# Optimization experiments

Hardware: AMD Instinct MI355X
Metric: run time of the kernel (lower is better)

The kernel has to match this reference:

```python
import jax, jax.numpy as jnp
import numpy as np
from jax import lax

IN_CH = 64
OUT_CH = 64
K = 3
CW = 2 * IN_CH + 49  # in_ch_weight = 2*in_ch + MAX_DISPLACEMENT**2 = 177
B = 8


def setup_inputs() -> dict:
    key = jax.random.key(0)
    ks = jax.random.split(key, 14)
    f = lambda k, s, sc: jax.random.normal(k, s, dtype=jnp.float32) * sc
    he5 = lambda cin: (2.0 / (cin * 25)) ** 0.5
    he3 = lambda cin: (2.0 / (cin * 9)) ** 0.5
    return {
        "x0": f(ks[0], (B, IN_CH, 128, 160), 1.0),
        "y0": f(ks[1], (B, IN_CH, 128, 160), 1.0),
        "x": f(ks[2], (B, IN_CH, 64, 80), 1.0),
        "y": f(ks[3], (B, IN_CH, 64, 80), 1.0),
        # weight-branch 0 (outputs CW channels)
        "w1a": f(ks[4], (IN_CH, CW, 5, 5), he5(CW)),
        "w1b": f(ks[5], (IN_CH, IN_CH, 5, 5), he5(IN_CH)),
        "w1c": f(ks[6], (CW, IN_CH, 3, 3), he3(IN_CH)),
        # weight-branch 1 / final (outputs OUT_CH channels)
        "w2a": f(ks[7], (IN_CH, CW, 5, 5), he5(CW)),
        "w2b": f(ks[8], (IN_CH, IN_CH, 5, 5), he5(IN_CH)),
        "w2c": f(ks[9], (OUT_CH, IN_CH, 3, 3), he3(IN_CH)),
        # grouped 1x1 dynamic-weight generators (per-channel affine maps)
        "wx_w": f(ks[10], (CW, CW * K * K), 0.05),
        "wx_b": f(ks[11], (CW, CW * K * K), 0.05),
        "wxf_w": f(ks[12], (OUT_CH, OUT_CH * K * K), 0.05),
        "wxf_b": f(ks[13], (OUT_CH, OUT_CH * K * K), 0.05),
    }


def _conv(x, w, stride, pad):
    return lax.conv_general_dilated(
        x, w, (stride, stride), [(pad, pad), (pad, pad)],
        dimension_numbers=("NCHW", "OIHW", "NCHW"))


def _pool2(x):
    b, c, h, w = x.shape
    return x.reshape(b, c, h // 2, 2, w // 2, 2).mean(axis=(3, 5))


def _corr(x0, y0):
    # FlowNet-style correlation: max_displacement=7, stride2=2 ->
    # displacements {-6,-4,-2,0,2,4,6}^2 = 49 channels; mean over C.
    b, c, h, w = x0.shape
    D = 6
    yp = jnp.pad(y0, ((0, 0), (0, 0), (D, D), (D, D)))
    outs = []
    for dy in range(-6, 7, 2):
        for dx in range(-6, 7, 2):
            ys = yp[:, :, D + dy:D + dy + h, D + dx:D + dx + w]
            outs.append(jnp.mean(x0 * ys, axis=1))
    return jnp.stack(outs, axis=1)  # [B, 49, H, W]


def _branch(feat, wa, wb, wc):
    h = jax.nn.relu(_conv(feat, wa, 2, 2))
    h = jax.nn.relu(_conv(h, wb, 2, 2))
    h = _conv(h, wc, 2, 1)
    return h.mean(axis=(2, 3))  # adaptive_avg_pool2d -> (1,1), squeezed: [B, Cout]


def _adaptive_conv(x, w, pad):
    # per-sample conv weights w: [B, Cout, Cin, k, k]
    def one(xb, wb):
        return _conv(xb[None], wb, 1, pad)[0]
    return jax.vmap(one)(x, w)


def reference(x0, y0, x, y, w1a, w1b, w1c, w2a, w2b, w2c, wx_w, wx_b, wxf_w, wxf_b):
    b = x.shape[0]
    x0p = _pool2(x0)
    y0p = _pool2(y0)
    corr = _corr(x0p, y0p)                      # [B, 49, H, W]
    feat = jnp.concatenate([corr, x, y], axis=1)  # [B, CW, H, W]

    # iteration 0 (N-1 = 1): generate per-sample [CW,CW,3,3] filters, apply
    fv = _branch(feat, w1a, w1b, w1c)           # [B, CW]
    wx = (fv[:, :, None] * wx_w[None] + wx_b[None]).reshape(b, CW, CW, K, K)
    feat = jax.nn.relu(_adaptive_conv(feat, wx, K // 2))

    # final: generate per-sample [OUT_CH,OUT_CH,3,3] filters and return them
    fv = _branch(feat, w2a, w2b, w2c)           # [B, OUT_CH]
    wxf = (fv[:, :, None] * wxf_w[None] + wxf_b[None]).reshape(b, OUT_CH, OUT_CH, K, K)
    return wxf
```

## Files before the change

kernel.cpp:

```cpp
#include <hip/hip_runtime.h>

typedef unsigned short u16;
typedef __attribute__((ext_vector_type(8))) short bf16x8;
typedef __attribute__((ext_vector_type(4))) float f32x4;
typedef _Float16 half2_t __attribute__((ext_vector_type(2)));

static constexpr int B  = 8;
static constexpr int C  = 64;
static constexpr int CW = 177;
static constexpr int H  = 64, W  = 80;
static constexpr int HP = 68, WP = 84, KC = 192;
static constexpr int PB = HP * WP * KC;
static constexpr int HA = 36, WA = 44;

__device__ __forceinline__ u16 f2b(float f) {
  union { float f; unsigned u; } v; v.f = f;
  unsigned u = v.u;
  return (u16)((u + 0x7FFF + ((u >> 16) & 1)) >> 16);
}
__device__ __forceinline__ u16 f2h(float f) {
  union { _Float16 h; u16 u; } v; v.h = (_Float16)f; return v.u;
}
__device__ __forceinline__ half2_t h2(unsigned u) {
  union { unsigned u; half2_t h; } v; v.u = u; return v.h;
}
__device__ __forceinline__ float blo(unsigned u) {
  union { unsigned v; float f; } t; t.v = u << 16; return t.f;
}
__device__ __forceinline__ float bhi(unsigned u) {
  union { unsigned v; float f; } t; t.v = u & 0xffff0000u; return t.f;
}
__device__ __forceinline__ unsigned pk2(u16 a, u16 b) {
  return (unsigned)a | ((unsigned)b << 16);
}

__global__ void setup_kernel(
    const float* __restrict__ w1a, const float* __restrict__ w2a,
    const float* __restrict__ w1b, const float* __restrict__ w2b,
    u16* __restrict__ A5a, u16* __restrict__ A5b,
    u16* __restrict__ A5b1, u16* __restrict__ A5b2,
    u16* __restrict__ featP1, u16* __restrict__ haP, u16* __restrict__ featP2) {
  int idx = blockIdx.x * blockDim.x + threadIdx.x;
  const int n0r = (B * PB) / 8;
  const int n1r = (B * HA * WA * 64) / 8;
  const int n2r = B * 592 * 24;
  const int s1 = 25 * 64 * 192, s2 = 25 * 64 * 64;
  bf16x8 z = 0;
  if (idx < n0r) { ((bf16x8*)featP1)[idx] = z; return; }
  idx -= n0r;
  if (idx < n1r) { ((bf16x8*)haP)[idx] = z; return; }
  idx -= n1r;
  if (idx < n2r) {
    int ch = idx % 24; int pi = (idx / 24) % 592; int b = idx / (24 * 592);
    int row, col;
    if (pi < 336) { int rr = pi / 84; row = (rr < 2) ? rr : rr + 64; col = pi % 84; }
    else { int pj = pi - 336; row = 2 + (pj >> 2); int cc = pj & 3; col = (cc < 2) ? cc : cc + 80; }
    *(bf16x8*)(featP2 + ((size_t)(b * HP + row) * WP + col) * KC + ch * 8) = z;
    return;
  }
  idx -= n2r;
  if (idx < 2 * s1) {
    const float* w = idx < s1 ? w1a : w2a; u16* A = idx < s1 ? A5a : A5b;
    int e = idx % s1;
    int j = e % 192; int i = (e / 192) % 64; int kk = e / (192 * 64);
    int ky = kk / 5, kx = kk % 5;
    float v = (j < CW) ? w[(((size_t)i * CW + j) * 5 + ky) * 5 + kx] : 0.f;
    A[e] = f2b(v);
    return;
  }
  idx -= 2 * s1;
  if (idx < 2 * s2) {
    const float* w = idx < s2 ? w1b : w2b; u16* A = idx < s2 ? A5b1 : A5b2;
    int e = idx % s2;
    int j = e % 64; int i = (e / 64) % 64; int kk = e / (64 * 64);
    int ky = kk / 5, kx = kk % 5;
    A[e] = f2b(w[(((size_t)i * 64 + j) * 5 + ky) * 5 + kx]);
  }
}

__global__ __launch_bounds__(256) void pool2_kernel(const float* __restrict__ x0, const float* __restrict__ y0,
                                                    u16* __restrict__ xpT, u16* __restrict__ ypT) {
  __shared__ u16 lt[80][66];
  int blk = blockIdx.x;
  int sel = blk & 1; int h = (blk >> 1) & 63; int b = blk >> 7;
  const float* in = sel ? y0 : x0;
  u16* out = sel ? ypT : xpT;
  int tid = threadIdx.x;
#pragma unroll
  for (int i = 0; i < 20; ++i) {
    int e = i * 256 + tid;
    int c = e / 80, w = e % 80;
    const float* p = in + ((size_t)(b * 64 + c) * 128 + 2 * h) * 160 + 2 * w;
    float2 r0 = *(const float2*)p;
    float2 r1 = *(const float2*)(p + 160);
    lt[w][c] = f2h(0.25f * (r0.x + r0.y + r1.x + r1.y));
  }
  __syncthreads();
#pragma unroll
  for (int i = 0; i < 20; ++i) {
    int e = i * 256 + tid;
    int w = e / 64, c = e % 64;
    out[((size_t)(b * H + h) * W + w) * C + c] = lt[w][c];
  }
}

__global__ __launch_bounds__(256) void corr_fill(const u16* __restrict__ xpT, const u16* __restrict__ ypT,
                                                 u16* __restrict__ featP) {
  int blk = blockIdx.x;
  int b = blk & 7; int inner = blk >> 3;
  int e = inner * 256 + threadIdx.x;
  int o = e % 49; int p = e / 49;
  int w = p % W; int h = p / W;
  int dy = (o / 7) * 2 - 6, dx = (o % 7) * 2 - 6;
  int hh = h + dy, ww = w + dx;
  float s = 0.f;
  if (hh >= 0 && hh < H && ww >= 0 && ww < W) {
    const uint4* xv = (const uint4*)(xpT + ((size_t)(b * H + h) * W + w) * C);
    const uint4* yv = (const uint4*)(ypT + ((size_t)(b * H + hh) * W + ww) * C);
#pragma unroll
    for (int i = 0; i < 8; ++i) {
      uint4 a = xv[i], q = yv[i];
      s = __builtin_amdgcn_fdot2(h2(a.x), h2(q.x), s, false);
      s = __builtin_amdgcn_fdot2(h2(a.y), h2(q.y), s, false);
      s = __builtin_amdgcn_fdot2(h2(a.z), h2(q.z), s, false);
      s = __builtin_amdgcn_fdot2(h2(a.w), h2(q.w), s, false);
    }
  }
  s *= (1.0f / 64.0f);
  featP[((size_t)(b * HP + h + 2) * WP + (w + 2)) * KC + o] = f2b(s);
}

__global__ __launch_bounds__(256) void copy_tr(const float* __restrict__ x, const float* __restrict__ y,
                                               u16* __restrict__ featP) {
  __shared__ float lt[40][129];
  int blk = blockIdx.x;
  int half = blk & 1; int h = (blk >> 1) & 63; int b = blk >> 7;
  int tid = threadIdx.x;
#pragma unroll
  for (int i = 0; i < 20; ++i) {
    int e = i * 256 + tid;
    int c2 = e / 40, w = e % 40;
    const float* src = (c2 < 64) ? x : y;
    int c = c2 & 63;
    lt[w][c2] = src[((size_t)(b * 64 + c) * H + h) * W + half * 40 + w];
  }
  __syncthreads();
#pragma unroll
  for (int i = 0; i < 20; ++i) {
    int e = i * 256 + tid;
    int wr = e / 128, c = e % 128;
    featP[((size_t)(b * HP + h + 2) * WP + (half * 40 + wr + 2)) * KC + 49 + c] = f2b(lt[wr][c]);
  }
}

__global__ void wx_pack(const float* __restrict__ fv, const float* __restrict__ ww,
                        const float* __restrict__ wb, u16* __restrict__ Apk) {
  int idx = blockIdx.x * blockDim.x + threadIdx.x;
  if (idx >= 9 * 192 * 24) return;
  int j8 = idx % 24; int i = (idx / 24) % 192; int kk = idx / (24 * 192);
  float wwv[8], wbv[8];
#pragma unroll
  for (int jj = 0; jj < 8; ++jj) {
    int j = j8 * 8 + jj;
    if (i < CW && j < CW) {
      size_t o = ((size_t)i * CW + j) * 9 + kk;
      wwv[jj] = ww[o]; wbv[jj] = wb[o];
    } else { wwv[jj] = 0.f; wbv[jj] = 0.f; }
  }
  int rb = i >> 4, il = i & 15;
  int c = j8 >> 3, rem = j8 & 7, half = rem >> 2, kqq = rem & 3;
  size_t dst = (((((size_t)kk * 12 + rb) * 3 + c) * 2 + half) * 64 + kqq * 16 + il) * 8;
  for (int b = 0; b < B; ++b) {
    float f = (i < CW) ? fv[b * CW + i] : 0.f;
    u16 o[8];
#pragma unroll
    for (int jj = 0; jj < 8; ++jj) o[jj] = f2b(f * wwv[jj] + wbv[jj]);
    uint4 v; v.x = pk2(o[0], o[1]); v.y = pk2(o[2], o[3]); v.z = pk2(o[4], o[5]); v.w = pk2(o[6], o[7]);
    *(uint4*)(Apk + (size_t)b * 331776 + dst) = v;
  }
}

__global__ __launch_bounds__(256, 2) void ad_conv_kernel(
    const u16* __restrict__ Apk, const u16* __restrict__ featP, u16* __restrict__ outP) {
  __shared__ u16 lds[2][84 * 64];
  int bid = (int)(blockIdx.x % 8) * 64 + (int)(blockIdx.x / 8);
  int h = bid & 63; int b = bid >> 6;
  int tid = threadIdx.x;
  int lane = tid & 63; int wm = tid >> 6;
  int l15 = lane & 15, kq = lane >> 4;

  f32x4 acc[3][5];
#pragma unroll
  for (int i = 0; i < 3; ++i)
#pragma unroll
    for (int j = 0; j < 5; ++j) acc[i][j] = (f32x4){0.f, 0.f, 0.f, 0.f};

  const u16* fb = featP + (size_t)b * PB;
  const u16* Ab = Apk + (size_t)b * 331776 + (size_t)lane * 8;

  int i0 = tid, i1 = tid + 256, i2 = tid + 512;
  int q0 = i0 >> 3, s0 = i0 & 7;
  int q1 = i1 >> 3, s1 = i1 & 7;
  int q2 = i2 >> 3, s2 = i2 & 7;
  int w0 = (i0 * 16) ^ ((q0 & 7) << 4);
  int w1 = (i1 * 16) ^ ((q1 & 7) << 4);
  int w2 = (i2 * 16) ^ ((q2 & 7) << 4);
  bool a2 = i2 < 672;

  bf16x8 r0, r1, r2;
  {
    const u16* g = fb + ((size_t)(h + 1) * WP) * KC;
    r0 = *(const bf16x8*)(g + (size_t)q0 * KC + s0 * 8);
    r1 = *(const bf16x8*)(g + (size_t)q1 * KC + s1 * 8);
    if (a2) r2 = *(const bf16x8*)(g + (size_t)q2 * KC + s2 * 8);
    char* lw = (char*)lds[0];
    *(bf16x8*)(lw + w0) = r0;
    *(bf16x8*)(lw + w1) = r1;
    if (a2) *(bf16x8*)(lw + w2) = r2;
  }
  __syncthreads();

#pragma unroll
  for (int s = 0; s < 9; ++s) {
    const int c = s / 3, ty = s % 3;
    if (s < 8) {
      const int cn = (s + 1) / 3, tyn = (s + 1) % 3;
      const u16* g = fb + ((size_t)(h + 1 + tyn) * WP) * KC + cn * 64;
      r0 = *(const bf16x8*)(g + (size_t)q0 * KC + s0 * 8);
      r1 = *(const bf16x8*)(g + (size_t)q1 * KC + s1 * 8);
      if (a2) r2 = *(const bf16x8*)(g + (size_t)q2 * KC + s2 * 8);
    }
    const char* lb = (const char*)lds[s & 1];
#pragma unroll
    for (int tx = 0; tx < 3; ++tx) {
      const int tap = ty * 3 + tx;
#pragma unroll
      for (int hk = 0; hk < 2; ++hk) {
        bf16x8 av[3], bv[5];
#pragma unroll
        for (int fm = 0; fm < 3; ++fm)
          av[fm] = *(const bf16x8*)(Ab + (size_t)(((tap * 12 + wm * 3 + fm) * 3 + c) * 2 + hk) * 512);
#pragma unroll
        for (int fn = 0; fn < 5; ++fn) {
          int q = fn * 16 + l15 + tx + 1;
          int byte = ((q * 8 + hk * 4 + kq) * 16) ^ ((q & 7) << 4);
          bv[fn] = *(const bf16x8*)(lb + byte);
        }
        __builtin_amdgcn_s_setprio(1);
#pragma unroll
        for (int fm = 0; fm < 3; ++fm)
#pragma unroll
          for (int fn = 0; fn < 5; ++fn)
            acc[fm][fn] = __builtin_amdgcn_mfma_f32_16x16x32_bf16(av[fm], bv[fn], acc[fm][fn], 0, 0, 0);
        __builtin_amdgcn_s_setprio(0);
      }
    }
    if (s < 8) {
      char* lw = (char*)lds[(s + 1) & 1];
      *(bf16x8*)(lw + w0) = r0;
      *(bf16x8*)(lw + w1) = r1;
      if (a2) *(bf16x8*)(lw + w2) = r2;
      __syncthreads();
    }
  }

#pragma unroll
  for (int fm = 0; fm < 3; ++fm) {
    int i0r = wm * 48 + fm * 16 + kq * 4;
#pragma unroll
    for (int fn = 0; fn < 5; ++fn) {
      int ow = fn * 16 + l15;
      u16* dst = outP + ((size_t)(b * HP + h + 2) * WP + (ow + 2)) * KC + i0r;
      uint2 pkv;
      pkv.x = pk2(f2b(fmaxf(acc[fm][fn][0], 0.f)), f2b(fmaxf(acc[fm][fn][1], 0.f)));
      pkv.y = pk2(f2b(fmaxf(acc[fm][fn][2], 0.f)), f2b(fmaxf(acc[fm][fn][3], 0.f)));
      *(uint2*)dst = pkv;
    }
  }
}

__global__ __launch_bounds__(128, 3) void conv5_split_kernel(
    const u16* __restrict__ A5, const u16* __restrict__ featP, u16* __restrict__ pa) {
  __shared__ u16 lds[2][84 * 64];
  int bid = (int)(blockIdx.x % 8) * 160 + (int)(blockIdx.x / 8);
  int rp = bid % 16; int ty = (bid / 16) % 5; int csel = (bid / 80) % 2; int b = bid / 160;
  int r0 = rp * 2;
  int kc0 = csel * 3;
  int tid = threadIdx.x;
  int lane = tid & 63; int wm = tid >> 6;
  int l15 = lane & 15, kq = lane >> 4;

  f32x4 acc[2][5];
#pragma unroll
  for (int i = 0; i < 2; ++i)
#pragma unroll
    for (int j = 0; j < 5; ++j) acc[i][j] = (f32x4){0.f, 0.f, 0.f, 0.f};

  const u16* fb = featP + (size_t)b * PB;
  int rowg0 = 2 * r0 + ty;

  bf16x8 r[6];
  auto load_chunk = [&](int kc) {
#pragma unroll
    for (int it = 0; it < 6; ++it) {
      int idx = it * 128 + tid;
      if (idx < 672) {
        int slot = idx & 3; int q = (idx >> 2) % 84; int row = idx / 336;
        r[it] = *(const bf16x8*)(fb + ((size_t)(rowg0 + 2 * row) * WP + q) * KC + kc * 32 + slot * 8);
      }
    }
  };
  auto write_chunk = [&](int buf) {
    char* lw = (char*)lds[buf];
#pragma unroll
    for (int it = 0; it < 6; ++it) {
      int idx = it * 128 + tid;
      if (idx < 672) {
        int q = (idx >> 2) % 84;
        int byte = (idx * 16) ^ ((q & 7) << 4);
        *(bf16x8*)(lw + byte) = r[it];
      }
    }
  };

  load_chunk(kc0);
  write_chunk(0);
  __syncthreads();

#pragma unroll
  for (int k = 0; k < 3; ++k) {
    int kc = kc0 + k;
    if (k < 2) load_chunk(kc + 1);
    const char* lb = (const char*)lds[k & 1];
#pragma unroll
    for (int tx = 0; tx < 5; ++tx) {
      bf16x8 av[2], bv[5];
#pragma unroll
      for (int fm = 0; fm < 2; ++fm)
        av[fm] = *(const bf16x8*)(A5 + ((size_t)((ty * 5 + tx) * 64 + wm * 32 + fm * 16 + l15)) * 192 + kc * 32 + kq * 8);
#pragma unroll
      for (int fn = 0; fn < 5; ++fn) {
        int p = fn * 16 + l15;
        int orow = p / 40, ocol = p % 40;
        int q = ocol * 2 + tx;
        int byte = (((orow * 84 + q) * 4 + kq) * 16) ^ ((q & 7) << 4);
        bv[fn] = *(const bf16x8*)(lb + byte);
      }
      __builtin_amdgcn_s_setprio(1);
#pragma unroll
      for (int fm = 0; fm < 2; ++fm)
#pragma unroll
        for (int fn = 0; fn < 5; ++fn)
          acc[fm][fn] = __builtin_amdgcn_mfma_f32_16x16x32_bf16(av[fm], bv[fn], acc[fm][fn], 0, 0, 0);
      __builtin_amdgcn_s_setprio(0);
    }
    if (k < 2) {
      write_chunk((k + 1) & 1);
      __syncthreads();
    }
  }
  int slot10 = csel * 5 + ty;
#pragma unroll
  for (int fm = 0; fm < 2; ++fm) {
    int oc0 = wm * 32 + fm * 16 + kq * 4;
#pragma unroll
    for (int fn = 0; fn < 5; ++fn) {
      int p = fn * 16 + l15;
      int orow = r0 + p / 40, ocol = p % 40;
      u16* dst = pa + (((((size_t)slot10 * B + b) * 32 + orow) * 40 + ocol) * 64) + oc0;
      uint2 pkv;
      pkv.x = pk2(f2b(acc[fm][fn][0]), f2b(acc[fm][fn][1]));
      pkv.y = pk2(f2b(acc[fm][fn][2]), f2b(acc[fm][fn][3]));
      *(uint2*)dst = pkv;
    }
  }
}

__global__ void combine10(const u16* __restrict__ pa, u16* __restrict__ haP) {
  int idx = blockIdx.x * blockDim.x + threadIdx.x;
  if (idx >= B * 32 * 40 * 8) return;
  int c8 = idx & 7; int t = idx >> 3;
  int ocol = t % 40; t /= 40; int orow = t % 32; int b = t / 32;
  float s[8];
#pragma unroll
  for (int k = 0; k < 8; ++k) s[k] = 0.f;
#pragma unroll
  for (int sl = 0; sl < 10; ++sl) {
    const u16* p = pa + ((((size_t)sl * B + b) * 32 + orow) * 40 + ocol) * 64 + c8 * 8;
    uint4 v = *(const uint4*)p;
    s[0] += blo(v.x); s[1] += bhi(v.x); s[2] += blo(v.y); s[3] += bhi(v.y);
    s[4] += blo(v.z); s[5] += bhi(v.z); s[6] += blo(v.w); s[7] += bhi(v.w);
  }
  uint4 o;
  o.x = pk2(f2b(fmaxf(s[0], 0.f)), f2b(fmaxf(s[1], 0.f)));
  o.y = pk2(f2b(fmaxf(s[2], 0.f)), f2b(fmaxf(s[3], 0.f)));
  o.z = pk2(f2b(fmaxf(s[4], 0.f)), f2b(fmaxf(s[5], 0.f)));
  o.w = pk2(f2b(fmaxf(s[6], 0.f)), f2b(fmaxf(s[7], 0.f)));
  *(uint4*)(haP + ((size_t)(b * HA + orow + 2) * WA + (ocol + 2)) * 64 + c8 * 8) = o;
}

template<int TY, int TX, int S, int OH, int OW, int M, int BM, int BN, int POFF,
         int KCIN, int HPIN, int WPIN>
__global__ __launch_bounds__(256) void gemm_conv(
    const u16* __restrict__ A, const u16* __restrict__ featP,
    float* __restrict__ outF, int MT, int NT) {
  constexpr int WM = BM / 2, WN = BN / 2, FM = WM / 16, FN = WN / 16;
  constexpr int NKC = KCIN / 32;
  int nwg = gridDim.x;
  int bid = (int)(blockIdx.x % 8) * (nwg / 8) + (int)(blockIdx.x / 8);
  int mt = bid % MT; int rest = bid / MT; int nt = rest % NT; int b = rest / NT;
  int lane = threadIdx.x & 63; int wv = threadIdx.x >> 6;
  int wm = wv >> 1, wn = wv & 1;
  int l15 = lane & 15, kq = lane >> 4;

  f32x4 acc[FM][FN];
#pragma unroll
  for (int i = 0; i < FM; ++i)
#pragma unroll
    for (int j = 0; j < FN; ++j) acc[i][j] = (f32x4){0.f, 0.f, 0.f, 0.f};

  const u16* Abase = A + (size_t)(mt * BM + wm * WM + l15) * KCIN + kq * 8;
  const u16* fb = featP + (size_t)b * (HPIN * WPIN * KCIN) + kq * 8;

  int ohh[FN], oww[FN];
#pragma unroll
  for (int fn = 0; fn < FN; ++fn) {
    int p = nt * BN + wn * WN + fn * 16 + l15;
    ohh[fn] = p / OW; oww[fn] = p % OW;
  }

  for (int kc = 0; kc < NKC; ++kc) {
    for (int ty = 0; ty < TY; ++ty)
      for (int tx = 0; tx < TX; ++tx) {
        const u16* At = Abase + (size_t)((ty * TX + tx) * M) * KCIN + kc * 32;
        bf16x8 av[FM], bv[FN];
#pragma unroll
        for (int fm = 0; fm < FM; ++fm)
          av[fm] = *(const bf16x8*)(At + fm * 16 * KCIN);
#pragma unroll
        for (int fn = 0; fn < FN; ++fn) {
          int hi = ohh[fn] * S + ty + POFF;
          int wi = oww[fn] * S + tx + POFF;
          bv[fn] = *(const bf16x8*)(fb + (size_t)(hi * WPIN + wi) * KCIN + kc * 32);
        }
#pragma unroll
        for (int fm = 0; fm < FM; ++fm)
#pragma unroll
          for (int fn = 0; fn < FN; ++fn)
            acc[fm][fn] = __builtin_amdgcn_mfma_f32_16x16x32_bf16(av[fm], bv[fn], acc[fm][fn], 0, 0, 0);
      }
  }

#pragma unroll
  for (int fm = 0; fm < FM; ++fm) {
    int oc0 = mt * BM + wm * WM + fm * 16 + kq * 4;
#pragma unroll
    for (int fn = 0; fn < FN; ++fn) {
#pragma unroll
      for (int r = 0; r < 4; ++r) {
        float v = fmaxf(acc[fm][fn][r], 0.f);
        outF[(((size_t)b * M + oc0 + r) * OH + ohh[fn]) * OW + oww[fn]] = v;
      }
    }
  }
}

__global__ void tapsum_kernel(const float* __restrict__ hb, float* __restrict__ Sm) {
  int b = blockIdx.x >> 6; int ic = blockIdx.x & 63; int lane = threadIdx.x;
  const float* p = hb + ((size_t)(b * 64 + ic)) * 320;
  float s[9];
#pragma unroll
  for (int t = 0; t < 9; ++t) s[t] = 0.f;
  for (int i = lane; i < 320; i += 64) {
    int ih = i / 20, iw = i % 20;
    float v = p[i];
#pragma unroll
    for (int ky = 0; ky < 3; ++ky) {
      int t2 = ih + 1 - ky;
      if (t2 < 0 || t2 > 14 || (t2 & 1)) continue;
#pragma unroll
      for (int kx = 0; kx < 3; ++kx) {
        int t3 = iw + 1 - kx;
        if (t3 < 0 || t3 > 18 || (t3 & 1)) continue;
        s[ky * 3 + kx] += v;
      }
    }
  }
#pragma unroll
  for (int t = 0; t < 9; ++t)
#pragma unroll
    for (int off = 32; off > 0; off >>= 1) s[t] += __shfl_down(s[t], off);
  if (lane == 0) {
#pragma unroll
    for (int t = 0; t < 9; ++t) Sm[(b * 64 + ic) * 9 + t] = s[t];
  }
}

__global__ void gemv_fv(const float* __restrict__ w3, const float* __restrict__ Sm,
                        float* __restrict__ fv, int OC) {
  int o = blockIdx.x % OC; int b = blockIdx.x / OC; int lane = threadIdx.x;
  const float* wp = w3 + ((size_t)o * 64 + lane) * 9;
  const float* sp = Sm + ((size_t)b * 64 + lane) * 9;
  float acc = 0.f;
#pragma unroll
  for (int t = 0; t < 9; ++t) acc += wp[t] * sp[t];
#pragma unroll
  for (int off = 32; off > 0; off >>= 1) acc += __shfl_down(acc, off);
  if (lane == 0) fv[b * OC + o] = acc * (1.0f / 80.0f);
}

__global__ void final_kernel(const float* __restrict__ fv, const float* __restrict__ ww,
                             const float* __restrict__ wb, float* __restrict__ out) {
  int idx = blockIdx.x * blockDim.x + threadIdx.x;
  if (idx >= B * 64 * 576) return;
  int kk = idx % 576; int i = (idx / 576) % 64; int b = idx / (576 * 64);
  out[idx] = fv[b * 64 + i] * ww[i * 576 + kk] + wb[i * 576 + kk];
}

extern "C" void kernel_launch(void* const* d_in, const int* in_sizes, int n_in,
                              void* d_out, int out_size, void* d_ws, size_t ws_size,
                              hipStream_t stream) {
  const float* x0    = (const float*)d_in[0];
  const float* y0    = (const float*)d_in[1];
  const float* x     = (const float*)d_in[2];
  const float* y     = (const float*)d_in[3];
  const float* w1a   = (const float*)d_in[4];
  const float* w1b   = (const float*)d_in[5];
  const float* w1c   = (const float*)d_in[6];
  const float* w2a   = (const float*)d_in[7];
  const float* w2b   = (const float*)d_in[8];
  const float* w2c   = (const float*)d_in[9];
  const float* wx_w  = (const float*)d_in[10];
  const float* wx_b  = (const float*)d_in[11];
  const float* wxf_w = (const float*)d_in[12];
  const float* wxf_b = (const float*)d_in[13];
  float* out = (float*)d_out;

  char* base = (char*)d_ws;
  size_t off = 0;
  auto take = [&](size_t bytes) -> char* {
    char* p = base + off; off += (bytes + 255) & ~(size_t)255; return p;
  };
  u16*   featP1 = (u16*)take((size_t)B * PB * 2);
  u16*   featP2 = (u16*)take((size_t)B * PB * 2);
  u16*   paAwx  = (u16*)take((size_t)10 * B * 32 * 40 * 64 * 2);
  u16*   pa     = paAwx;
  u16*   Apk    = paAwx;
  u16*   xpT    = paAwx;
  u16*   ypT    = paAwx + (size_t)B * H * W * C;
  u16*   A5a    = (u16*)take((size_t)25 * 64 * 192 * 2);
  u16*   A5b    = (u16*)take((size_t)25 * 64 * 192 * 2);
  u16*   A5b1   = (u16*)take((size_t)25 * 64 * 64 * 2);
  u16*   A5b2   = (u16*)take((size_t)25 * 64 * 64 * 2);
  u16*   haP    = (u16*)take((size_t)B * HA * WA * 64 * 2);
  float* hb     = (float*)take((size_t)B * 64 * 320 * 4);
  float* Sm     = (float*)take((size_t)B * 64 * 9 * 4);
  float* fv1    = (float*)take((size_t)B * CW * 4);
  float* fv2    = (float*)take((size_t)B * 64 * 4);
  if (off > ws_size) return;

  const int TB = 256;

  {
    int n = (B * PB) / 8 + (B * HA * WA * 64) / 8 + B * 592 * 24
          + 2 * 25 * 64 * 192 + 2 * 25 * 64 * 64;
    setup_kernel<<<(n + TB - 1) / TB, TB, 0, stream>>>(
        w1a, w2a, w1b, w2b, A5a, A5b, A5b1, A5b2, featP1, haP, featP2);
  }
  pool2_kernel<<<B * 64 * 2, TB, 0, stream>>>(x0, y0, xpT, ypT);
  corr_fill<<<8 * 980, TB, 0, stream>>>(xpT, ypT, featP1);
  copy_tr<<<B * 64 * 2, TB, 0, stream>>>(x, y, featP1);

  conv5_split_kernel<<<1280, 128, 0, stream>>>(A5a, featP1, pa);
  combine10<<<(B * 32 * 40 * 8 + TB - 1) / TB, TB, 0, stream>>>(pa, haP);
  gemm_conv<5, 5, 2, 16, 20, 64, 32, 32, 0, 64, HA, WA>
      <<<160, TB, 0, stream>>>(A5b1, haP, hb, 2, 10);
  tapsum_kernel<<<B * 64, 64, 0, stream>>>(hb, Sm);
  gemv_fv<<<B * CW, 64, 0, stream>>>(w1c, Sm, fv1, CW);

  wx_pack<<<(9 * 192 * 24 + TB - 1) / TB, TB, 0, stream>>>(fv1, wx_w, wx_b, Apk);
  ad_conv_kernel<<<64 * B, 256, 0, stream>>>(Apk, featP1, featP2);

  conv5_split_kernel<<<1280, 128, 0, stream>>>(A5b, featP2, pa);
  combine10<<<(B * 32 * 40 * 8 + TB - 1) / TB, TB, 0, stream>>>(pa, haP);
  gemm_conv<5, 5, 2, 16, 20, 64, 32, 32, 0, 64, HA, WA>
      <<<160, TB, 0, stream>>>(A5b2, haP, hb, 2, 10);
  tapsum_kernel<<<B * 64, 64, 0, stream>>>(hb, Sm);
  gemv_fv<<<B * 64, 64, 0, stream>>>(w2c, Sm, fv2, 64);

  final_kernel<<<(B * 64 * 576 + TB - 1) / TB, TB, 0, stream>>>(fv2, wxf_w, wxf_b, out);
}
```

Before: 201.9 us.

## Fuse small kernels and fold tap-sum into gemm epilogue via atomics

Merges pool2 into the setup kernel, and corr_fill with copy_tr, so each pair runs as one launch with block-index dispatch. The tapsum pass is replaced by atomic accumulation into Sm in the gemm_conv epilogue, with Sm zeroed in combine10, and the final gemv is fused with the output affine kernel. The aim is to cut launch count and the hb intermediate round-trip. The cost is atomic contention, nondeterministic summation order, and a dependency on zeroing Sm inside combine10. The epilogue also assumes FM=FN=1, which holds for the 32x32 tiles used.

```diff
diff --git a/kernel.cpp b/kernel.cpp
--- a/kernel.cpp
+++ b/kernel.cpp
@@ -34,13 +34,40 @@
   return (unsigned)a | ((unsigned)b << 16);
 }
 
-__global__ void setup_kernel(
+__global__ __launch_bounds__(256) void setup_pool(
+    const float* __restrict__ x0, const float* __restrict__ y0,
+    u16* __restrict__ xpT, u16* __restrict__ ypT,
     const float* __restrict__ w1a, const float* __restrict__ w2a,
     const float* __restrict__ w1b, const float* __restrict__ w2b,
     u16* __restrict__ A5a, u16* __restrict__ A5b,
     u16* __restrict__ A5b1, u16* __restrict__ A5b2,
     u16* __restrict__ featP1, u16* __restrict__ haP, u16* __restrict__ featP2) {
-  int idx = blockIdx.x * blockDim.x + threadIdx.x;
+  __shared__ u16 lt[80][66];
+  int blk0 = blockIdx.x;
+  int tid = threadIdx.x;
+  if (blk0 < 1024) {
+    int sel = blk0 & 1; int h = (blk0 >> 1) & 63; int b = blk0 >> 7;
+    const float* in = sel ? y0 : x0;
+    u16* out = sel ? ypT : xpT;
+#pragma unroll
+    for (int i = 0; i < 20; ++i) {
+      int e = i * 256 + tid;
+      int c = e / 80, w = e % 80;
+      const float* p = in + ((size_t)(b * 64 + c) * 128 + 2 * h) * 160 + 2 * w;
+      float2 r0 = *(const float2*)p;
+      float2 r1 = *(const float2*)(p + 160);
+      lt[w][c] = f2h(0.25f * (r0.x + r0.y + r1.x + r1.y));
+    }
+    __syncthreads();
+#pragma unroll
+    for (int i = 0; i < 20; ++i) {
+      int e = i * 256 + tid;
+      int w = e / 64, c = e % 64;
+      out[((size_t)(b * H + h) * W + w) * C + c] = lt[w][c];
+    }
+    return;
+  }
+  int idx = (blk0 - 1024) * 256 + tid;
   const int n0r = (B * PB) / 8;
   const int n1r = (B * HA * WA * 64) / 8;
   const int n2r = B * 592 * 24;
@@ -78,64 +105,40 @@
   }
 }
 
-__global__ __launch_bounds__(256) void pool2_kernel(const float* __restrict__ x0, const float* __restrict__ y0,
-                                                    u16* __restrict__ xpT, u16* __restrict__ ypT) {
-  __shared__ u16 lt[80][66];
-  int blk = blockIdx.x;
-  int sel = blk & 1; int h = (blk >> 1) & 63; int b = blk >> 7;
-  const float* in = sel ? y0 : x0;
-  u16* out = sel ? ypT : xpT;
+__global__ __launch_bounds__(256) void corr_copy(
+    const u16* __restrict__ xpT, const u16* __restrict__ ypT,
+    const float* __restrict__ x, const float* __restrict__ y,
+    u16* __restrict__ featP) {
+  __shared__ float smf[40 * 129];
+  int blk0 = blockIdx.x;
   int tid = threadIdx.x;
-#pragma unroll
-  for (int i = 0; i < 20; ++i) {
-    int e = i * 256 + tid;
-    int c = e / 80, w = e % 80;
-    const float* p = in + ((size_t)(b * 64 + c) * 128 + 2 * h) * 160 + 2 * w;
-    float2 r0 = *(const float2*)p;
-    float2 r1 = *(const float2*)(p + 160);
-    lt[w][c] = f2h(0.25f * (r0.x + r0.y + r1.x + r1.y));
-  }
-  __syncthreads();
-#pragma unroll
-  for (int i = 0; i < 20; ++i) {
-    int e = i * 256 + tid;
-    int w = e / 64, c = e % 64;
-    out[((size_t)(b * H + h) * W + w) * C + c] = lt[w][c];
-  }
-}
-
-__global__ __launch_bounds__(256) void corr_fill(const u16* __restrict__ xpT, const u16* __restrict__ ypT,
-                                                 u16* __restrict__ featP) {
-  int blk = blockIdx.x;
-  int b = blk & 7; int inner = blk >> 3;
-  int e = inner * 256 + threadIdx.x;
-  int o = e % 49; int p = e / 49;
-  int w = p % W; int h = p / W;
-  int dy = (o / 7) * 2 - 6, dx = (o % 7) * 2 - 6;
-  int hh = h + dy, ww = w + dx;
-  float s = 0.f;
-  if (hh >= 0 && hh < H && ww >= 0 && ww < W) {
-    const uint4* xv = (const uint4*)(xpT + ((size_t)(b * H + h) * W + w) * C);
-    const uint4* yv = (const uint4*)(ypT + ((size_t)(b * H + hh) * W + ww) * C);
-#pragma unroll
-    for (int i = 0; i < 8; ++i) {
-      uint4 a = xv[i], q = yv[i];
-      s = __builtin_amdgcn_fdot2(h2(a.x), h2(q.x), s, false);
-      s = __builtin_amdgcn_fdot2(h2(a.y), h2(q.y), s, false);
-      s = __builtin_amdgcn_fdot2(h2(a.z), h2(q.z), s, false);
-      s = __builtin_amdgcn_fdot2(h2(a.w), h2(q.w), s, false);
-    }
-  }
-  s *= (1.0f / 64.0f);
-  featP[((size_t)(b * HP + h + 2) * WP + (w + 2)) * KC + o] = f2b(s);
-}
-
-__global__ __launch_bounds__(256) void copy_tr(const float* __restrict__ x, const float* __restrict__ y,
-                                               u16* __restrict__ featP) {
-  __shared__ float lt[40][129];
-  int blk = blockIdx.x;
+  if (blk0 < 7840) {
+    int b = blk0 & 7; int inner = blk0 >> 3;
+    int e = inner * 256 + tid;
+    int o = e % 49; int p = e / 49;
+    int w = p % W; int h = p / W;
+    int dy = (o / 7) * 2 - 6, dx = (o % 7) * 2 - 6;
+    int hh = h + dy, ww = w + dx;
+    float s = 0.f;
+    if (hh >= 0 && hh < H && ww >= 0 && ww < W) {
+      const uint4* xv = (const uint4*)(xpT + ((size_t)(b * H + h) * W + w) * C);
+      const uint4* yv = (const uint4*)(ypT + ((size_t)(b * H + hh) * W + ww) * C);
+#pragma unroll
+      for (int i = 0; i < 8; ++i) {
+        uint4 a = xv[i], q = yv[i];
+        s = __builtin_amdgcn_fdot2(h2(a.x), h2(q.x), s, false);
+        s = __builtin_amdgcn_fdot2(h2(a.y), h2(q.y), s, false);
+        s = __builtin_amdgcn_fdot2(h2(a.z), h2(q.z), s, false);
+        s = __builtin_amdgcn_fdot2(h2(a.w), h2(q.w), s, false);
+      }
+    }
+    s *= (1.0f / 64.0f);
+    featP[((size_t)(b * HP + h + 2) * WP + (w + 2)) * KC + o] = f2b(s);
+    return;
+  }
+  int blk = blk0 - 7840;
+  float (*lt)[129] = (float(*)[129])smf;
   int half = blk & 1; int h = (blk >> 1) & 63; int b = blk >> 7;
-  int tid = threadIdx.x;
 #pragma unroll
   for (int i = 0; i < 20; ++i) {
     int e = i * 256 + tid;
@@ -376,8 +379,10 @@
   }
 }
 
-__global__ void combine10(const u16* __restrict__ pa, u16* __restrict__ haP) {
+__global__ void combine10(const u16* __restrict__ pa, u16* __restrict__ haP,
+                          float* __restrict__ Sm) {
   int idx = blockIdx.x * blockDim.x + threadIdx.x;
+  if (idx < B * 64 * 9) Sm[idx] = 0.f;
   if (idx >= B * 32 * 40 * 8) return;
   int c8 = idx & 7; int t = idx >> 3;
   int ocol = t % 40; t /= 40; int orow = t % 32; int b = t / 32;
@@ -401,9 +406,9 @@
 
 template<int TY, int TX, int S, int OH, int OW, int M, int BM, int BN, int POFF,
          int KCIN, int HPIN, int WPIN>
-__global__ __launch_bounds__(256) void gemm_conv(
+__global__ __launch_bounds__(256) void gemm_conv_ts(
     const u16* __restrict__ A, const u16* __restrict__ featP,
-    float* __restrict__ outF, int MT, int NT) {
+    float* __restrict__ Sm, int MT, int NT) {
   constexpr int WM = BM / 2, WN = BN / 2, FM = WM / 16, FN = WN / 16;
   constexpr int NKC = KCIN / 32;
   int nwg = gridDim.x;
@@ -451,48 +456,27 @@
       }
   }
 
-#pragma unroll
-  for (int fm = 0; fm < FM; ++fm) {
-    int oc0 = mt * BM + wm * WM + fm * 16 + kq * 4;
-#pragma unroll
-    for (int fn = 0; fn < FN; ++fn) {
-#pragma unroll
-      for (int r = 0; r < 4; ++r) {
-        float v = fmaxf(acc[fm][fn][r], 0.f);
-        outF[(((size_t)b * M + oc0 + r) * OH + ohh[fn]) * OW + oww[fn]] = v;
-      }
-    }
-  }
-}
-
-__global__ void tapsum_kernel(const float* __restrict__ hb, float* __restrict__ Sm) {
-  int b = blockIdx.x >> 6; int ic = blockIdx.x & 63; int lane = threadIdx.x;
-  const float* p = hb + ((size_t)(b * 64 + ic)) * 320;
-  float s[9];
-#pragma unroll
-  for (int t = 0; t < 9; ++t) s[t] = 0.f;
-  for (int i = lane; i < 320; i += 64) {
-    int ih = i / 20, iw = i % 20;
-    float v = p[i];
-#pragma unroll
-    for (int ky = 0; ky < 3; ++ky) {
-      int t2 = ih + 1 - ky;
-      if (t2 < 0 || t2 > 14 || (t2 & 1)) continue;
-#pragma unroll
-      for (int kx = 0; kx < 3; ++kx) {
-        int t3 = iw + 1 - kx;
-        if (t3 < 0 || t3 > 18 || (t3 & 1)) continue;
-        s[ky * 3 + kx] += v;
-      }
-    }
-  }
-#pragma unroll
-  for (int t = 0; t < 9; ++t)
-#pragma unroll
-    for (int off = 32; off > 0; off >>= 1) s[t] += __shfl_down(s[t], off);
-  if (lane == 0) {
-#pragma unroll
-    for (int t = 0; t < 9; ++t) Sm[(b * 64 + ic) * 9 + t] = s[t];
+  int oh = ohh[0], ow = oww[0];
+  int oc0 = mt * BM + wm * WM + kq * 4;
+  float v0 = fmaxf(acc[0][0][0], 0.f);
+  float v1 = fmaxf(acc[0][0][1], 0.f);
+  float v2 = fmaxf(acc[0][0][2], 0.f);
+  float v3 = fmaxf(acc[0][0][3], 0.f);
+  float* sb0 = Sm + ((size_t)(b * 64 + oc0)) * 9;
+#pragma unroll
+  for (int ky = 0; ky < 3; ++ky) {
+    int t2 = oh + 1 - ky;
+    if (t2 < 0 || t2 > 14 || (t2 & 1)) continue;
+#pragma unroll
+    for (int kx = 0; kx < 3; ++kx) {
+      int t3 = ow + 1 - kx;
+      if (t3 < 0 || t3 > 18 || (t3 & 1)) continue;
+      int t = ky * 3 + kx;
+      atomicAdd(sb0 + t, v0);
+      atomicAdd(sb0 + 9 + t, v1);
+      atomicAdd(sb0 + 18 + t, v2);
+      atomicAdd(sb0 + 27 + t, v3);
+    }
   }
 }
 
@@ -509,12 +493,24 @@
   if (lane == 0) fv[b * OC + o] = acc * (1.0f / 80.0f);
 }
 
-__global__ void final_kernel(const float* __restrict__ fv, const float* __restrict__ ww,
-                             const float* __restrict__ wb, float* __restrict__ out) {
-  int idx = blockIdx.x * blockDim.x + threadIdx.x;
-  if (idx >= B * 64 * 576) return;
-  int kk = idx % 576; int i = (idx / 576) % 64; int b = idx / (576 * 64);
-  out[idx] = fv[b * 64 + i] * ww[i * 576 + kk] + wb[i * 576 + kk];
+__global__ void gemv_final(const float* __restrict__ w3, const float* __restrict__ Sm,
+                           const float* __restrict__ ww, const float* __restrict__ wb,
+                           float* __restrict__ out) {
+  int o = blockIdx.x & 63; int b = blockIdx.x >> 6; int lane = threadIdx.x;
+  const float* wp = w3 + ((size_t)o * 64 + lane) * 9;
+  const float* sp = Sm + ((size_t)b * 64 + lane) * 9;
+  float acc = 0.f;
+#pragma unroll
+  for (int t = 0; t < 9; ++t) acc += wp[t] * sp[t];
+#pragma unroll
+  for (int off = 32; off > 0; off >>= 1) acc += __shfl_down(acc, off);
+  float fvv = __shfl(acc, 0) * (1.0f / 80.0f);
+  const float* wwp = ww + (size_t)o * 576;
+  const float* wbp = wb + (size_t)o * 576;
+  float* op = out + ((size_t)(b * 64 + o)) * 576;
+#pragma unroll
+  for (int k = 0; k < 9; ++k)
+    op[k * 64 + lane] = fvv * wwp[k * 64 + lane] + wbp[k * 64 + lane];
 }
 
 extern "C" void kernel_launch(void* const* d_in, const int* in_sizes, int n_in,
@@ -553,40 +549,33 @@
   u16*   A5b1   = (u16*)take((size_t)25 * 64 * 64 * 2);
   u16*   A5b2   = (u16*)take((size_t)25 * 64 * 64 * 2);
   u16*   haP    = (u16*)take((size_t)B * HA * WA * 64 * 2);
-  float* hb     = (float*)take((size_t)B * 64 * 320 * 4);
   float* Sm     = (float*)take((size_t)B * 64 * 9 * 4);
   float* fv1    = (float*)take((size_t)B * CW * 4);
-  float* fv2    = (float*)take((size_t)B * 64 * 4);
   if (off > ws_size) return;
 
   const int TB = 256;
 
   {
-    int n = (B * PB) / 8 + (B * HA * WA * 64) / 8 + B * 592 * 24
-          + 2 * 25 * 64 * 192 + 2 * 25 * 64 * 64;
-    setup_kernel<<<(n + TB - 1) / TB, TB, 0, stream>>>(
+    int nsetup = (B * PB) / 8 + (B * HA * WA * 64) / 8 + B * 592 * 24
+               + 2 * 25 * 64 * 192 + 2 * 25 * 64 * 64;
+    int grid = 1024 + (nsetup + TB - 1) / TB;
+    setup_pool<<<grid, TB, 0, stream>>>(x0, y0, xpT, ypT,
         w1a, w2a, w1b, w2b, A5a, A5b, A5b1, A5b2, featP1, haP, featP2);
   }
-  pool2_kernel<<<B * 64 * 2, TB, 0, stream>>>(x0, y0, xpT, ypT);
-  corr_fill<<<8 * 980, TB, 0, stream>>>(xpT, ypT, featP1);
-  copy_tr<<<B * 64 * 2, TB, 0, stream>>>(x, y, featP1);
+  corr_copy<<<7840 + 1024, TB, 0, stream>>>(xpT, ypT, x, y, featP1);
 
   conv5_split_kernel<<<1280, 128, 0, stream>>>(A5a, featP1, pa);
-  combine10<<<(B * 32 * 40 * 8 + TB - 1) / TB, TB, 0, stream>>>(pa, haP);
-  gemm_conv<5, 5, 2, 16, 20, 64, 32, 32, 0, 64, HA, WA>
-      <<<160, TB, 0, stream>>>(A5b1, haP, hb, 2, 10);
-  tapsum_kernel<<<B * 64, 64, 0, stream>>>(hb, Sm);
+  combine10<<<(B * 32 * 40 * 8 + TB - 1) / TB, TB, 0, stream>>>(pa, haP, Sm);
+  gemm_conv_ts<5, 5, 2, 16, 20, 64, 32, 32, 0, 64, HA, WA>
+      <<<160, TB, 0, stream>>>(A5b1, haP, Sm, 2, 10);
   gemv_fv<<<B * CW, 64, 0, stream>>>(w1c, Sm, fv1, CW);
 
   wx_pack<<<(9 * 192 * 24 + TB - 1) / TB, TB, 0, stream>>>(fv1, wx_w, wx_b, Apk);
   ad_conv_kernel<<<64 * B, 256, 0, stream>>>(Apk, featP1, featP2);
 
   conv5_split_kernel<<<1280, 128, 0, stream>>>(A5b, featP2, pa);
-  combine10<<<(B * 32 * 40 * 8 + TB - 1) / TB, TB, 0, stream>>>(pa, haP);
-  gemm_conv<5, 5, 2, 16, 20, 64, 32, 32, 0, 64, HA, WA>
-      <<<160, TB, 0, stream>>>(A5b2, haP, hb, 2, 10);
-  tapsum_kernel<<<B * 64, 64, 0, stream>>>(hb, Sm);
-  gemv_fv<<<B * 64, 64, 0, stream>>>(w2c, Sm, fv2, 64);
-
-  final_kernel<<<(B * 64 * 576 + TB - 1) / TB, TB, 0, stream>>>(fv2, wxf_w, wxf_b, out);
-}
+  combine10<<<(B * 32 * 40 * 8 + TB - 1) / TB, TB, 0, stream>>>(pa, haP, Sm);
+  gemm_conv_ts<5, 5, 2, 16, 20, 64, 32, 32, 0, 64, HA, WA>
+      <<<160, TB, 0, stream>>>(A5b2, haP, Sm, 2, 10);
+  gemv_final<<<B * 64, 64, 0, stream>>>(w2c, Sm, wxf_w, wxf_b, out);
+}
```

Result: slower. 277.2 us (+37.3%).
